# Optimization experiments

Measured on AMD Instinct MI355X. Metric: run time of the kernel, lower is better.

Reference implementation:

```python
import jax, jax.numpy as jnp
import numpy as np


def _chunk_indices(cu_seqlens, kernel_size, kernel_stride):
    """Host-side (static) computation of ragged strided chunk gather indices,
    mirroring calc_chunks_with_stride in the torch source. cu_seqlens is
    integer metadata (constant w.r.t. differentiation / kernel work)."""
    cu = np.asarray(cu_seqlens, dtype=np.int64)
    lens = cu[1:] - cu[:-1]                      # per-sequence lengths [B]
    max_len = int(lens.max())
    max_c = max(0, (max_len - kernel_size) // kernel_stride + 1)
    offs = np.arange(max_c, dtype=np.int64) * kernel_stride      # [C]
    starts = cu[:-1, None] + offs[None, :]                        # [B, C]
    valid = (offs[None, :] + kernel_size) <= lens[:, None]        # [B, C]
    valid_starts = starts[valid]                                  # [N]
    # [N, kernel_size] token indices into k for every valid chunk
    idx = valid_starts[:, None] + np.arange(kernel_size, dtype=np.int64)[None, :]
    cu_comp = np.zeros(len(cu), dtype=np.int32)
    cu_comp[1:] = np.cumsum(valid.sum(axis=1))
    return jnp.asarray(idx, dtype=jnp.int32), jnp.asarray(cu_comp)


def setup_inputs() -> dict:
    key = jax.random.key(0)
    total_tokens, num_heads_k, head_dim = 32768, 4, 128
    k = jax.random.normal(key, (total_tokens, num_heads_k, head_dim), dtype=jnp.float32)
    # 4 sequences of 8192 tokens each (ragged layout, here equal lengths)
    cu_seqlens = jnp.array([0, 8192, 16384, 24576, 32768], dtype=jnp.int32)
    return {"k": k, "cu_seqlens": cu_seqlens, "kernel_size": 32, "kernel_stride": 16}


def reference(k, cu_seqlens, kernel_size, kernel_stride):
    # k: [total_tokens, H, D]
    idx, cu_seqlens_compressed = _chunk_indices(cu_seqlens, kernel_size, kernel_stride)
    gathered = k[idx]                    # [num_chunks, kernel_size, H, D]
    compressed_k = gathered.mean(axis=1)  # mean-pool within each chunk -> [num_chunks, H, D]
    return compressed_k, cu_seqlens_compressed
```

## Files before the change

### kernel.cpp

```cpp
#include <hip/hip_runtime.h>


#define HD 512
#define HD4 (HD / 4)

__global__ void meta_kernel(const int* __restrict__ cu, int B,
                            const int* __restrict__ ks_p,
                            const int* __restrict__ kst_p,
                            int* __restrict__ meta,
                            float* __restrict__ out_tail) {
    if (threadIdx.x == 0 && blockIdx.x == 0) {
        int ks = ks_p[0];
        int kst = kst_p[0];
        int acc = 0;
        meta[1] = 0;
        out_tail[0] = 0.0f;
        for (int b = 0; b < B; ++b) {
            int len = cu[b + 1] - cu[b];
            int nc = (len >= ks) ? ((len - ks) / kst + 1) : 0;
            acc += nc;
            meta[2 + b] = acc;
            out_tail[b + 1] = (float)acc;
        }
        meta[0] = acc;
    }
}

__global__ __launch_bounds__(128)
void pool_kernel(const float* __restrict__ k,
                 const int* __restrict__ cu,
                 const int* __restrict__ ks_p,
                 const int* __restrict__ kst_p,
                 const int* __restrict__ meta,
                 float* __restrict__ out, int B) {
    const int total = meta[0];
    const int ks = ks_p[0];
    const int kst = kst_p[0];
    const float inv = 1.0f / (float)ks;
    const int tid = threadIdx.x;

    for (int c = blockIdx.x; c < total; c += gridDim.x) {
        int b = 0;
        while (b + 1 < B && meta[1 + b + 1] <= c) ++b;
        const int lc = c - meta[1 + b];
        const int start = cu[b] + lc * kst;

        const float4* __restrict__ src =
            (const float4*)k + (size_t)start * HD4 + tid;
        float4 acc = make_float4(0.f, 0.f, 0.f, 0.f);
        for (int t = 0; t < ks; ++t) {
            float4 v = src[(size_t)t * HD4];
            acc.x += v.x; acc.y += v.y; acc.z += v.z; acc.w += v.w;
        }
        acc.x *= inv; acc.y *= inv; acc.z *= inv; acc.w *= inv;
        ((float4*)out)[(size_t)c * HD4 + tid] = acc;
    }
}

extern "C" void kernel_launch(void* const* d_in, const int* in_sizes, int n_in,
                              void* d_out, int out_size, void* d_ws, size_t ws_size,
                              hipStream_t stream) {
    const float* k   = (const float*)d_in[0];
    const int*   cu  = (const int*)d_in[1];
    const int*   ksp = (const int*)d_in[2];
    const int*   kstp= (const int*)d_in[3];
    float* out = (float*)d_out;
    int*   meta = (int*)d_ws;

    const int B = in_sizes[1] - 1;
    float* out_tail = out + (out_size - (B + 1));

    meta_kernel<<<1, 64, 0, stream>>>(cu, B, ksp, kstp, meta, out_tail);

    pool_kernel<<<2048, 128, 0, stream>>>(k, cu, ksp, kstp, meta, out, B);
}
```

Baseline: 110.4 us.

## Fuse metadata into pooling kernel, split chunk rows across two thread halves, swizzle blocks

Removes the separate single-thread metadata kernel: every block recomputes the chunk totals from cu_seqlens, and block 0 writes the compressed cu_seqlens tail. The pooling block grows to 256 threads, and each half sums half of the chunk's rows before a shared-memory reduction, giving more loads in flight per chunk. Block-to-chunk assignment is swizzled across groups of 8 so that consecutive blocks touch different regions of k, which could change L2 and XCD locality. The cost is extra per-block scalar work and two barriers per chunk.

```diff
diff --git a/kernel.cpp b/kernel.cpp
--- a/kernel.cpp
+++ b/kernel.cpp
@@ -1,76 +1,91 @@
 #include <hip/hip_runtime.h>
 
 
-#define HD 512
-#define HD4 (HD / 4)
+#define HD4 128
 
-__global__ void meta_kernel(const int* __restrict__ cu, int B,
-                            const int* __restrict__ ks_p,
-                            const int* __restrict__ kst_p,
-                            int* __restrict__ meta,
-                            float* __restrict__ out_tail) {
-    if (threadIdx.x == 0 && blockIdx.x == 0) {
-        int ks = ks_p[0];
-        int kst = kst_p[0];
+__global__ __launch_bounds__(256)
+void compress_k_fused(const float* __restrict__ k,
+                      const int* __restrict__ cu,
+                      const int* __restrict__ ks_p,
+                      const int* __restrict__ kst_p,
+                      float* __restrict__ out,
+                      int B, int out_size) {
+    const int ks  = ks_p[0];
+    const int kst = kst_p[0];
+    const float inv = 1.0f / (float)ks;
+
+    int total = 0;
+    for (int b = 0; b < B; ++b) {
+        int len = cu[b + 1] - cu[b];
+        total += (len >= ks) ? ((len - ks) / kst + 1) : 0;
+    }
+
+    const int tid = threadIdx.x;
+
+    if (blockIdx.x == 0 && tid <= B) {
         int acc = 0;
-        meta[1] = 0;
-        out_tail[0] = 0.0f;
-        for (int b = 0; b < B; ++b) {
+        for (int b = 0; b < tid; ++b) {
+            int len = cu[b + 1] - cu[b];
+            acc += (len >= ks) ? ((len - ks) / kst + 1) : 0;
+        }
+        out[(size_t)out_size - (B + 1) + tid] = (float)acc;
+    }
+
+    const int col  = tid & (HD4 - 1);
+    const int half = tid >> 7;
+    __shared__ float4 red[HD4];
+
+    const int nwg = gridDim.x;
+    const int cpx = nwg >> 3;
+    const int swz = (blockIdx.x & 7) * cpx + (blockIdx.x >> 3);
+
+    for (int c = swz; c < total; c += nwg) {
+        int b = 0, pre = 0;
+        for (;;) {
             int len = cu[b + 1] - cu[b];
             int nc = (len >= ks) ? ((len - ks) / kst + 1) : 0;
-            acc += nc;
-            meta[2 + b] = acc;
-            out_tail[b + 1] = (float)acc;
+            if (c < pre + nc) break;
+            pre += nc; ++b;
         }
-        meta[0] = acc;
-    }
-}
+        const int start = cu[b] + (c - pre) * kst;
 
-__global__ __launch_bounds__(128)
-void pool_kernel(const float* __restrict__ k,
-                 const int* __restrict__ cu,
-                 const int* __restrict__ ks_p,
-                 const int* __restrict__ kst_p,
-                 const int* __restrict__ meta,
-                 float* __restrict__ out, int B) {
-    const int total = meta[0];
-    const int ks = ks_p[0];
-    const int kst = kst_p[0];
-    const float inv = 1.0f / (float)ks;
-    const int tid = threadIdx.x;
-
-    for (int c = blockIdx.x; c < total; c += gridDim.x) {
-        int b = 0;
-        while (b + 1 < B && meta[1 + b + 1] <= c) ++b;
-        const int lc = c - meta[1 + b];
-        const int start = cu[b] + lc * kst;
+        const int r0 = half ? (ks >> 1) : 0;
+        const int r1 = half ? ks : (ks >> 1);
 
         const float4* __restrict__ src =
-            (const float4*)k + (size_t)start * HD4 + tid;
+            (const float4*)k + (size_t)(start + r0) * HD4 + col;
         float4 acc = make_float4(0.f, 0.f, 0.f, 0.f);
-        for (int t = 0; t < ks; ++t) {
-            float4 v = src[(size_t)t * HD4];
+        #pragma unroll 4
+        for (int t = r0; t < r1; ++t) {
+            float4 v = *src;
+            src += HD4;
             acc.x += v.x; acc.y += v.y; acc.z += v.z; acc.w += v.w;
         }
-        acc.x *= inv; acc.y *= inv; acc.z *= inv; acc.w *= inv;
-        ((float4*)out)[(size_t)c * HD4 + tid] = acc;
+
+        if (half) red[col] = acc;
+        __syncthreads();
+        if (!half) {
+            float4 o = red[col];
+            o.x = (acc.x + o.x) * inv;
+            o.y = (acc.y + o.y) * inv;
+            o.z = (acc.z + o.z) * inv;
+            o.w = (acc.w + o.w) * inv;
+            ((float4*)out)[(size_t)c * HD4 + col] = o;
+        }
+        __syncthreads();
     }
 }
 
 extern "C" void kernel_launch(void* const* d_in, const int* in_sizes, int n_in,
                               void* d_out, int out_size, void* d_ws, size_t ws_size,
                               hipStream_t stream) {
-    const float* k   = (const float*)d_in[0];
-    const int*   cu  = (const int*)d_in[1];
-    const int*   ksp = (const int*)d_in[2];
-    const int*   kstp= (const int*)d_in[3];
+    const float* k    = (const float*)d_in[0];
+    const int*   cu   = (const int*)d_in[1];
+    const int*   ksp  = (const int*)d_in[2];
+    const int*   kstp = (const int*)d_in[3];
     float* out = (float*)d_out;
-    int*   meta = (int*)d_ws;
 
     const int B = in_sizes[1] - 1;
-    float* out_tail = out + (out_size - (B + 1));
 
-    meta_kernel<<<1, 64, 0, stream>>>(cu, B, ksp, kstp, meta, out_tail);
-
-    pool_kernel<<<2048, 128, 0, stream>>>(k, cu, ksp, kstp, meta, out, B);
+    compress_k_fused<<<2048, 256, 0, stream>>>(k, cu, ksp, kstp, out, B, out_size);
 }
```

Result: faster. 101.1 us (-8.5%).
